# Performance work log

Measured on AMD Instinct MI355X. Metric: run time of the kernel, lower is better.

Reference implementation:

```python
import jax, jax.numpy as jnp
import numpy as np

D_MODEL = 1024
N_HEAD = 16
D_K = D_MODEL // N_HEAD
D_FF = 2048
N_EXPERTS = 8
TOP_K = 2
B = 4
S = 1024
LN_EPS = 1e-5


def _layer_norm(x, g, b):
    mu = jnp.mean(x, axis=-1, keepdims=True)
    var = jnp.mean(jnp.square(x - mu), axis=-1, keepdims=True)
    return (x - mu) * jax.lax.rsqrt(var + LN_EPS) * g + b


def setup_inputs() -> dict:
    key = jax.random.key(0)
    ks = jax.random.split(key, 16)
    std = 0.02
    inp = {
        "x": jax.random.normal(ks[0], (B, S, D_MODEL), dtype=jnp.float32),
        "mask": jnp.ones((B, S, S), dtype=jnp.int32),
        "ln1_g": jnp.ones((D_MODEL,), jnp.float32),
        "ln1_b": jnp.zeros((D_MODEL,), jnp.float32),
        "wq": jax.random.normal(ks[1], (D_MODEL, D_MODEL), jnp.float32) * std,
        "wk": jax.random.normal(ks[2], (D_MODEL, D_MODEL), jnp.float32) * std,
        "wv": jax.random.normal(ks[3], (D_MODEL, D_MODEL), jnp.float32) * std,
        "wo": jax.random.normal(ks[4], (D_MODEL, D_MODEL), jnp.float32) * std,
        "wqd": jax.random.normal(ks[5], (D_MODEL, D_MODEL), jnp.float32) * std,
        "wkd": jax.random.normal(ks[6], (D_MODEL, D_MODEL), jnp.float32) * std,
        "wvd": jax.random.normal(ks[7], (D_MODEL, D_MODEL), jnp.float32) * std,
        "wod": jax.random.normal(ks[8], (D_MODEL, D_MODEL), jnp.float32) * std,
        "w_gate": jax.random.normal(ks[9], (D_MODEL, 2), jnp.float32) * std,
        "ln2_g": jnp.ones((D_MODEL,), jnp.float32),
        "ln2_b": jnp.zeros((D_MODEL,), jnp.float32),
        "w_router": jax.random.normal(ks[10], (D_MODEL, N_EXPERTS), jnp.float32) * std,
        "e_w1": jax.random.normal(ks[11], (N_EXPERTS, D_MODEL, D_FF), jnp.float32) * std,
        "e_w2": jax.random.normal(ks[12], (N_EXPERTS, D_FF, D_MODEL), jnp.float32) * std,
    }
    return inp


def _attention(x, mask, wq, wk, wv, wo, wqd, wkd, wvd, wod, w_gate):
    b, s, d = x.shape

    def split_heads(t):  # [b,s,d] -> [b,h,s,dk]
        return t.reshape(b, s, N_HEAD, D_K).transpose(0, 2, 1, 3)

    def merge_heads(t):  # [b,h,s,dk] -> [b,s,d]
        return t.transpose(0, 2, 1, 3).reshape(b, s, d)

    # dense attention branch
    q = split_heads(x @ wq)
    k = split_heads(x @ wk)
    v = split_heads(x @ wv)
    scores = jnp.einsum("bhqd,bhkd->bhqk", q, k) / jnp.sqrt(jnp.float32(D_K))
    scores = jnp.where(mask[:, None, :, :] == 0, jnp.float32(-1e9), scores)
    probs = jax.nn.softmax(scores, axis=-1)
    dense = merge_heads(jnp.einsum("bhqk,bhkd->bhqd", probs, v)) @ wo

    # linear delta attention branch (O(n))
    qd = split_heads(x @ wqd)
    kd = split_heads(x @ wkd)
    vd = split_heads(x @ wvd)
    q_lin = jax.nn.relu(qd)
    k_lin = jax.nn.relu(kd)
    # NOTE: original uses the *non-relu* k for the context matrix
    context = jnp.einsum("bhsd,bhse->bhde", kd, vd)  # [b,h,dk,dk]
    out = jnp.einsum("bhsd,bhde->bhse", q_lin, context)
    z = jnp.sum(q_lin * jnp.sum(k_lin, axis=-2, keepdims=True), axis=-1, keepdims=True) + 1e-6
    delta = merge_heads(out / z) @ wod

    gate = jax.nn.softmax(x @ w_gate, axis=-1)  # [b,s,2]
    return gate[..., 0:1] * dense + gate[..., 1:2] * delta


def _moe(x, w_router, e_w1, e_w2):
    b, s, d = x.shape
    xt = x.reshape(b * s, d)  # tokens
    logits = xt @ w_router  # [N, E]
    topk_logits, topk_idx = jax.lax.top_k(logits, TOP_K)
    topk_w = jax.nn.softmax(topk_logits, axis=-1)  # [N, K]
    # dense combine weights [N, E] (equivalent to masked gather/scatter-add)
    n = xt.shape[0]
    comb = jnp.zeros((n, N_EXPERTS), xt.dtype).at[jnp.arange(n)[:, None], topk_idx].add(topk_w)
    # all tokens through all experts (jit-friendly dense dispatch)
    h = jax.nn.gelu(jnp.einsum("nd,edf->enf", xt, e_w1), approximate=False)
    y = jnp.einsum("enf,efd->end", h, e_w2)
    out = jnp.einsum("end,ne->nd", y, comb)
    return out.reshape(b, s, d)


def reference(x, mask, ln1_g, ln1_b, wq, wk, wv, wo, wqd, wkd, wvd, wod, w_gate,
              ln2_g, ln2_b, w_router, e_w1, e_w2):
    x = x + _attention(_layer_norm(x, ln1_g, ln1_b), mask,
                       wq, wk, wv, wo, wqd, wkd, wvd, wod, w_gate)
    x = x + _moe(_layer_norm(x, ln2_g, ln2_b), w_router, e_w1, e_w2)
    return x
```

## Files before the change

kernel.cpp:

```cpp
#include <hip/hip_runtime.h>
#include <stdint.h>


typedef __attribute__((ext_vector_type(8))) short short8;
typedef __attribute__((ext_vector_type(4))) float floatx4;

#define DMODEL 1024
#define SEQ    1024
#define NHEAD  16
#define DK     64
#define DFF    2048
#define NEXP   8
#define MAXTILE 144

__device__ __forceinline__ float bf2f(unsigned short h){
  union{unsigned u;float f;}v; v.u=((unsigned)h)<<16; return v.f;
}
__device__ __forceinline__ unsigned short f2bf(float f){
  union{float f;unsigned u;}v; v.f=f;
  unsigned r=(v.u + 0x7FFFu + ((v.u>>16)&1u))>>16; return (unsigned short)r;
}
__device__ __forceinline__ void splitbf(float v, unsigned short& hi, unsigned short& lo){
  hi = f2bf(v); lo = f2bf(v - bf2f(hi));
}

__device__ __forceinline__ void glds16(const unsigned short* g, unsigned short* l){
  __builtin_amdgcn_global_load_lds(
      (const __attribute__((address_space(1))) void*)g,
      (__attribute__((address_space(3))) void*)l, 16, 0, 0);
}

__device__ __forceinline__ float block_sum(float v, float* red){
  for(int off=32;off;off>>=1) v += __shfl_down(v,off,64);
  int w = threadIdx.x>>6;
  __syncthreads();
  if((threadIdx.x&63)==0) red[w]=v;
  __syncthreads();
  return red[0]+red[1]+red[2]+red[3];
}

__global__ __launch_bounds__(256) void k_maskpack(
    const int* __restrict__ mask, unsigned long long* __restrict__ mp){
  int gw = blockIdx.x*4 + (threadIdx.x>>6);
  int lane = threadIdx.x&63;
  unsigned long long bm = __ballot(mask[(long)gw*64 + lane] != 0);
  if(lane==0) mp[gw]=bm;
}

__global__ __launch_bounds__(256) void k_transpose_f2(
    const float* __restrict__ src, unsigned short* __restrict__ dh,
    unsigned short* __restrict__ dl, long srs, long drs, long sbs, long dbs){
  __shared__ float t[32][33];
  src += (long)blockIdx.z*sbs; dh += (long)blockIdx.z*dbs; dl += (long)blockIdx.z*dbs;
  int c0 = blockIdx.x*32, r0 = blockIdx.y*32;
  int tx = threadIdx.x & 31, ty = threadIdx.x >> 5;
  for(int i=0;i<32;i+=8)
    t[ty+i][tx] = src[(long)(r0+ty+i)*srs + (c0+tx)];
  __syncthreads();
  for(int i=0;i<32;i+=8){
    unsigned short hi,lo; splitbf(t[tx][ty+i],hi,lo);
    long idx = (long)(c0+ty+i)*drs + (r0+tx);
    dh[idx]=hi; dl[idx]=lo;
  }
}

__global__ __launch_bounds__(256) void k_transpose_f(
    const float* __restrict__ src, unsigned short* __restrict__ dst,
    long srs, long drs, long sbs, long dbs){
  __shared__ float t[32][33];
  src += (long)blockIdx.z*sbs; dst += (long)blockIdx.z*dbs;
  int c0 = blockIdx.x*32, r0 = blockIdx.y*32;
  int tx = threadIdx.x & 31, ty = threadIdx.x >> 5;
  for(int i=0;i<32;i+=8)
    t[ty+i][tx] = src[(long)(r0+ty+i)*srs + (c0+tx)];
  __syncthreads();
  for(int i=0;i<32;i+=8)
    dst[(long)(c0+ty+i)*drs + (r0+tx)] = f2bf(t[tx][ty+i]);
}

__global__ __launch_bounds__(256) void k_vt(
    const unsigned short* __restrict__ qh, const unsigned short* __restrict__ ql,
    unsigned short* __restrict__ vth, unsigned short* __restrict__ vtl, long coff){
  __shared__ unsigned short th[32][33], tl[32][33];
  int z = blockIdx.z, b = z>>4, h = z&15;
  int s0 = blockIdx.x*32, d0 = blockIdx.y*32;
  int tx = threadIdx.x & 31, ty = threadIdx.x >> 5;
  for(int i=0;i<32;i+=8){
    long src = (long)(b*SEQ + s0+ty+i)*6144 + coff + h*DK + d0+tx;
    th[ty+i][tx] = qh[src]; tl[ty+i][tx] = ql[src];
  }
  __syncthreads();
  for(int i=0;i<32;i+=8){
    long dst = ((long)z*DK + d0+ty+i)*SEQ + s0+tx;
    vth[dst] = th[tx][ty+i]; vtl[dst] = tl[tx][ty+i];
  }
}

__global__ __launch_bounds__(256) void k_ln1(
    const float* __restrict__ x, const float* __restrict__ g,
    const float* __restrict__ b, unsigned short* __restrict__ oh,
    unsigned short* __restrict__ ol){
  __shared__ float red[4];
  int t = blockIdx.x, tid = threadIdx.x;
  long base = (long)t*DMODEL + tid*4;
  floatx4 xv = *(const floatx4*)(x + base);
  float v[4] = {xv[0], xv[1], xv[2], xv[3]};
  float s = block_sum(v[0]+v[1]+v[2]+v[3], red);
  float mu = s * (1.f/DMODEL);
  float q=0.f;
  for(int i=0;i<4;i++){ float d=v[i]-mu; q+=d*d; }
  q = block_sum(q, red);
  float inv = rsqrtf(q*(1.f/DMODEL) + 1e-5f);
  for(int i=0;i<4;i++){
    int d = tid*4+i;
    unsigned short hi,lo; splitbf((v[i]-mu)*inv*g[d] + b[d], hi, lo);
    oh[base+i]=hi; ol[base+i]=lo;
  }
}

template<int SPLIT>
__global__ __launch_bounds__(256) void k_gemm128_ss(
    const unsigned short* __restrict__ Ah, const unsigned short* __restrict__ Al,
    const unsigned short* __restrict__ Bh, const unsigned short* __restrict__ Bl,
    unsigned short* __restrict__ Ch, unsigned short* __restrict__ Cl,
    float* __restrict__ Cf, int K, int lda, int ldb, int ldc, int gridN){
  __shared__ unsigned short Ash[128*32], Asl[128*32];
  __shared__ unsigned short Bsh[128*32], Bsl[128*32];
  int nwg = gridDim.x, bid = blockIdx.x;
  int swz = (bid & 7)*(nwg >> 3) + (bid >> 3);
  int bx = swz % gridN, by = swz / gridN;
  int m0 = by*128, n0 = bx*128;
  int tid = threadIdx.x, w = tid>>6, lane = tid&63;
  int qm = lane&15, quad = lane>>4;
  int wr = w>>1, wc = w&1;
  int lg = lane>>3, pp = lane&7, px = pp ^ lg;
  int rowl = (w<<4) + (lg<<1) + (px>>2);
  int c4s = (px&3)*8;
  int sdst = w*512 + lane*8;
  const unsigned short* pA0h = Ah + (long)(m0+rowl   )*lda + c4s;
  const unsigned short* pA1h = Ah + (long)(m0+rowl+64)*lda + c4s;
  const unsigned short* pA0l = Al + (long)(m0+rowl   )*lda + c4s;
  const unsigned short* pA1l = Al + (long)(m0+rowl+64)*lda + c4s;
  const unsigned short* pB0h = Bh + (long)(n0+rowl   )*ldb + c4s;
  const unsigned short* pB1h = Bh + (long)(n0+rowl+64)*ldb + c4s;
  const unsigned short* pB0l = Bl + (long)(n0+rowl   )*ldb + c4s;
  const unsigned short* pB1l = Bl + (long)(n0+rowl+64)*ldb + c4s;
  int fc = (((((qm&1)<<2)|quad) ^ (qm>>1))<<3);

  floatx4 acc[4][4];
  #pragma unroll
  for(int m=0;m<4;m++)
    #pragma unroll
    for(int n=0;n<4;n++) acc[m][n] = (floatx4){0.f,0.f,0.f,0.f};

  for(int k0=0;k0<K;k0+=32){
    __syncthreads();
    glds16(pA0h+k0, Ash+sdst); glds16(pA1h+k0, Ash+sdst+2048);
    glds16(pA0l+k0, Asl+sdst); glds16(pA1l+k0, Asl+sdst+2048);
    glds16(pB0h+k0, Bsh+sdst); glds16(pB1h+k0, Bsh+sdst+2048);
    glds16(pB0l+k0, Bsl+sdst); glds16(pB1l+k0, Bsl+sdst+2048);
    __syncthreads();
    short8 ah[4], al[4], bh[4], bl[4];
    #pragma unroll
    for(int m=0;m<4;m++){
      int ar = (wr*32 + m*8 + (qm>>1))*64 + fc;
      ah[m] = *(const short8*)(Ash+ar);
      al[m] = *(const short8*)(Asl+ar);
    }
    #pragma unroll
    for(int n=0;n<4;n++){
      int br = (wc*32 + n*8 + (qm>>1))*64 + fc;
      bh[n] = *(const short8*)(Bsh+br);
      bl[n] = *(const short8*)(Bsl+br);
    }
    #pragma unroll
    for(int m=0;m<4;m++)
      #pragma unroll
      for(int n=0;n<4;n++){
        acc[m][n] = __builtin_amdgcn_mfma_f32_16x16x32_bf16(ah[m],bh[n],acc[m][n],0,0,0);
        acc[m][n] = __builtin_amdgcn_mfma_f32_16x16x32_bf16(ah[m],bl[n],acc[m][n],0,0,0);
        acc[m][n] = __builtin_amdgcn_mfma_f32_16x16x32_bf16(al[m],bh[n],acc[m][n],0,0,0);
      }
  }
  #pragma unroll
  for(int m=0;m<4;m++){
    int row = m0 + wr*64 + m*16 + quad*4;
    #pragma unroll
    for(int r=0;r<4;r++){
      long rb = (long)(row+r)*ldc + n0 + wc*64;
      #pragma unroll
      for(int n=0;n<4;n++){
        float v = acc[m][n][r];
        if(SPLIT){
          unsigned short hi,lo; splitbf(v,hi,lo);
          Ch[rb+n*16+qm]=hi; Cl[rb+n*16+qm]=lo;
        }else{
          Cf[rb+n*16+qm]=v;
        }
      }
    }
  }
}

__global__ __launch_bounds__(256) void k_gate(
    const unsigned short* __restrict__ hh, const unsigned short* __restrict__ hl,
    const float* __restrict__ wg, float* __restrict__ gates){
  int token = blockIdx.x*4 + (threadIdx.x>>6);
  int lane = threadIdx.x&63;
  long hb = (long)token*DMODEL + lane*16;
  const float* w = wg + lane*16*2;
  float s0=0.f, s1=0.f;
  for(int i=0;i<16;i++){
    float hv = bf2f(hh[hb+i]) + bf2f(hl[hb+i]);
    s0 += hv*w[2*i]; s1 += hv*w[2*i+1];
  }
  for(int off=32;off;off>>=1){ s0+=__shfl_down(s0,off,64); s1+=__shfl_down(s1,off,64); }
  if(lane==0){
    float m=fmaxf(s0,s1), e0=__expf(s0-m), e1=__expf(s1-m), inv=1.f/(e0+e1);
    gates[token*2]=e0*inv; gates[token*2+1]=e1*inv;
  }
}

__global__ __launch_bounds__(256) void k_attn_flash3(
    const unsigned short* __restrict__ qh, const unsigned short* __restrict__ qlp,
    const unsigned short* __restrict__ vth, const unsigned short* __restrict__ vtl,
    const unsigned long long* __restrict__ mp, unsigned short* __restrict__ dmh,
    unsigned short* __restrict__ dml){
  __shared__ unsigned short Ksh[64*64], Ksl[64*64];
  __shared__ unsigned short Vsh[64*64], Vsl[64*64];
  __shared__ unsigned short PWh[4*16*64], PWl[4*16*64];
  int bh = blockIdx.y, b = bh>>4, h = bh&15;
  int tid = threadIdx.x, w = tid>>6, lane = tid&63;
  int qm = lane&15, quad = (lane>>4)&3;
  int q0 = blockIdx.x*64 + w*16;
  long qrow = (long)(b*SEQ+q0+qm)*6144 + h*DK;
  short8 a_qh0 = *(const short8*)(qh +qrow+quad*8);
  short8 a_qh1 = *(const short8*)(qh +qrow+32+quad*8);
  short8 a_ql0 = *(const short8*)(qlp+qrow+quad*8);
  short8 a_ql1 = *(const short8*)(qlp+qrow+32+quad*8);
  float m[4], l[4];
  floatx4 o0={0,0,0,0}, o1={0,0,0,0}, o2={0,0,0,0}, o3={0,0,0,0};
  #pragma unroll
  for(int r=0;r<4;r++){ m[r]=-3.0e38f; l[r]=0.f; }
  const unsigned long long* mrow = mp + ((long)b*SEQ + q0 + quad*4)*16;

  int r8 = lane>>3;
  int c8 = (lane&7) ^ r8;
  int d0 = w*512 + lane*8;
  const unsigned short* pKh0 = qh  + (long)(b*SEQ + w*8 + r8)*6144 + 1024 + h*DK + c8*8;
  const unsigned short* pKl0 = qlp + (long)(b*SEQ + w*8 + r8)*6144 + 1024 + h*DK + c8*8;
  const unsigned short* pKh1 = pKh0 + 32L*6144;
  const unsigned short* pKl1 = pKl0 + 32L*6144;
  const unsigned short* pVh0 = vth + ((long)bh*DK + w*8 + r8)*SEQ + c8*8;
  const unsigned short* pVl0 = vtl + ((long)bh*DK + w*8 + r8)*SEQ + c8*8;
  const unsigned short* pVh1 = pVh0 + 32L*SEQ;
  const unsigned short* pVl1 = pVl0 + 32L*SEQ;
  int q7 = qm&7;

  for(int kt=0; kt<SEQ; kt+=64){
    __syncthreads();
    long ko = (long)kt*6144;
    glds16(pKh0+ko, Ksh+d0); glds16(pKh1+ko, Ksh+d0+2048);
    glds16(pKl0+ko, Ksl+d0); glds16(pKl1+ko, Ksl+d0+2048);
    glds16(pVh0+kt, Vsh+d0); glds16(pVh1+kt, Vsh+d0+2048);
    glds16(pVl0+kt, Vsl+d0); glds16(pVl1+kt, Vsl+d0+2048);
    __syncthreads();

    int wd = kt>>6;
    unsigned long long mws[4] = {mrow[wd], mrow[16+wd], mrow[32+wd], mrow[48+wd]};
    floatx4 s[4];
    #pragma unroll
    for(int st=0;st<4;st++){
      int krow = (st*16+qm)*64;
      short8 kh0 = *(const short8*)(Ksh + krow + ((quad    ^q7)<<3));
      short8 kh1 = *(const short8*)(Ksh + krow + (((4|quad)^q7)<<3));
      short8 kl0 = *(const short8*)(Ksl + krow + ((quad    ^q7)<<3));
      short8 kl1 = *(const short8*)(Ksl + krow + (((4|quad)^q7)<<3));
      floatx4 acc = {0,0,0,0};
      acc = __builtin_amdgcn_mfma_f32_16x16x32_bf16(a_qh0,kh0,acc,0,0,0);
      acc = __builtin_amdgcn_mfma_f32_16x16x32_bf16(a_qh1,kh1,acc,0,0,0);
      acc = __builtin_amdgcn_mfma_f32_16x16x32_bf16(a_qh0,kl0,acc,0,0,0);
      acc = __builtin_amdgcn_mfma_f32_16x16x32_bf16(a_qh1,kl1,acc,0,0,0);
      acc = __builtin_amdgcn_mfma_f32_16x16x32_bf16(a_ql0,kh0,acc,0,0,0);
      acc = __builtin_amdgcn_mfma_f32_16x16x32_bf16(a_ql1,kh1,acc,0,0,0);
      s[st] = acc;
    }
    #pragma unroll
    for(int r=0;r<4;r++){
      float v0 = ((mws[r]>>(   qm))&1) ? s[0][r]*0.125f : -1e9f;
      float v1 = ((mws[r]>>(16+qm))&1) ? s[1][r]*0.125f : -1e9f;
      float v2 = ((mws[r]>>(32+qm))&1) ? s[2][r]*0.125f : -1e9f;
      float v3 = ((mws[r]>>(48+qm))&1) ? s[3][r]*0.125f : -1e9f;
      float tm = fmaxf(fmaxf(v0,v1), fmaxf(v2,v3));
      tm = fmaxf(tm, __shfl_xor(tm,1,16));
      tm = fmaxf(tm, __shfl_xor(tm,2,16));
      tm = fmaxf(tm, __shfl_xor(tm,4,16));
      tm = fmaxf(tm, __shfl_xor(tm,8,16));
      float nm = fmaxf(m[r], tm);
      float al = __expf(m[r]-nm);
      m[r] = nm;
      float p0=__expf(v0-nm), p1=__expf(v1-nm), p2=__expf(v2-nm), p3=__expf(v3-nm);
      float rs = p0+p1+p2+p3;
      rs += __shfl_xor(rs,1,16); rs += __shfl_xor(rs,2,16);
      rs += __shfl_xor(rs,4,16); rs += __shfl_xor(rs,8,16);
      l[r] = l[r]*al + rs;
      o0[r]*=al; o1[r]*=al; o2[r]*=al; o3[r]*=al;
      int row = quad*4+r, rsw = row&7;
      int pb = w*1024 + row*64 + (qm&7);
      unsigned short hi,lo;
      splitbf(p0,hi,lo); PWh[pb + ((( (qm>>3))^rsw)<<3)]=hi; PWl[pb + ((( (qm>>3))^rsw)<<3)]=lo;
      splitbf(p1,hi,lo); PWh[pb + (((2|(qm>>3))^rsw)<<3)]=hi; PWl[pb + (((2|(qm>>3))^rsw)<<3)]=lo;
      splitbf(p2,hi,lo); PWh[pb + (((4|(qm>>3))^rsw)<<3)]=hi; PWl[pb + (((4|(qm>>3))^rsw)<<3)]=lo;
      splitbf(p3,hi,lo); PWh[pb + (((6|(qm>>3))^rsw)<<3)]=hi; PWl[pb + (((6|(qm>>3))^rsw)<<3)]=lo;
    }
    __builtin_amdgcn_wave_barrier();
    int prb = w*1024 + qm*64;
    short8 ph0 = *(const short8*)(PWh + prb + ((quad    ^q7)<<3));
    short8 ph1 = *(const short8*)(PWh + prb + (((4|quad)^q7)<<3));
    short8 pl0 = *(const short8*)(PWl + prb + ((quad    ^q7)<<3));
    short8 pl1 = *(const short8*)(PWl + prb + (((4|quad)^q7)<<3));
    __builtin_amdgcn_wave_barrier();
    {
      int c0 = (quad    ^q7)<<3;
      int c1 = ((4|quad)^q7)<<3;
      int vr0 = (0*16+qm)*64, vr1 = (1*16+qm)*64, vr2 = (2*16+qm)*64, vr3 = (3*16+qm)*64;
      short8 v0h0=*(const short8*)(Vsh+vr0+c0), v0h1=*(const short8*)(Vsh+vr0+c1);
      short8 v1h0=*(const short8*)(Vsh+vr1+c0), v1h1=*(const short8*)(Vsh+vr1+c1);
      short8 v2h0=*(const short8*)(Vsh+vr2+c0), v2h1=*(const short8*)(Vsh+vr2+c1);
      short8 v3h0=*(const short8*)(Vsh+vr3+c0), v3h1=*(const short8*)(Vsh+vr3+c1);
      short8 v0l0=*(const short8*)(Vsl+vr0+c0), v0l1=*(const short8*)(Vsl+vr0+c1);
      short8 v1l0=*(const short8*)(Vsl+vr1+c0), v1l1=*(const short8*)(Vsl+vr1+c1);
      short8 v2l0=*(const short8*)(Vsl+vr2+c0), v2l1=*(const short8*)(Vsl+vr2+c1);
      short8 v3l0=*(const short8*)(Vsl+vr3+c0), v3l1=*(const short8*)(Vsl+vr3+c1);
      o0 = __builtin_amdgcn_mfma_f32_16x16x32_bf16(ph0,v0h0,o0,0,0,0);
      o0 = __builtin_amdgcn_mfma_f32_16x16x32_bf16(ph1,v0h1,o0,0,0,0);
      o0 = __builtin_amdgcn_mfma_f32_16x16x32_bf16(ph0,v0l0,o0,0,0,0);
      o0 = __builtin_amdgcn_mfma_f32_16x16x32_bf16(ph1,v0l1,o0,0,0,0);
      o0 = __builtin_amdgcn_mfma_f32_16x16x32_bf16(pl0,v0h0,o0,0,0,0);
      o0 = __builtin_amdgcn_mfma_f32_16x16x32_bf16(pl1,v0h1,o0,0,0,0);
      o1 = __builtin_amdgcn_mfma_f32_16x16x32_bf16(ph0,v1h0,o1,0,0,0);
      o1 = __builtin_amdgcn_mfma_f32_16x16x32_bf16(ph1,v1h1,o1,0,0,0);
      o1 = __builtin_amdgcn_mfma_f32_16x16x32_bf16(ph0,v1l0,o1,0,0,0);
      o1 = __builtin_amdgcn_mfma_f32_16x16x32_bf16(ph1,v1l1,o1,0,0,0);
      o1 = __builtin_amdgcn_mfma_f32_16x16x32_bf16(pl0,v1h0,o1,0,0,0);
      o1 = __builtin_amdgcn_mfma_f32_16x16x32_bf16(pl1,v1h1,o1,0,0,0);
      o2 = __builtin_amdgcn_mfma_f32_16x16x32_bf16(ph0,v2h0,o2,0,0,0);
      o2 = __builtin_amdgcn_mfma_f32_16x16x32_bf16(ph1,v2h1,o2,0,0,0);
      o2 = __builtin_amdgcn_mfma_f32_16x16x32_bf16(ph0,v2l0,o2,0,0,0);
      o2 = __builtin_amdgcn_mfma_f32_16x16x32_bf16(ph1,v2l1,o2,0,0,0);
      o2 = __builtin_amdgcn_mfma_f32_16x16x32_bf16(pl0,v2h0,o2,0,0,0);
      o2 = __builtin_amdgcn_mfma_f32_16x16x32_bf16(pl1,v2h1,o2,0,0,0);
      o3 = __builtin_amdgcn_mfma_f32_16x16x32_bf16(ph0,v3h0,o3,0,0,0);
      o3 = __builtin_amdgcn_mfma_f32_16x16x32_bf16(ph1,v3h1,o3,0,0,0);
      o3 = __builtin_amdgcn_mfma_f32_16x16x32_bf16(ph0,v3l0,o3,0,0,0);
      o3 = __builtin_amdgcn_mfma_f32_16x16x32_bf16(ph1,v3l1,o3,0,0,0);
      o3 = __builtin_amdgcn_mfma_f32_16x16x32_bf16(pl0,v3h0,o3,0,0,0);
      o3 = __builtin_amdgcn_mfma_f32_16x16x32_bf16(pl1,v3h1,o3,0,0,0);
    }
  }
  #pragma unroll
  for(int r=0;r<4;r++){
    float inv = 1.f/l[r];
    long rb = ((long)(b*SEQ + q0 + quad*4 + r))*DMODEL + h*DK;
    unsigned short hi,lo;
    splitbf(o0[r]*inv,hi,lo); dmh[rb+   qm]=hi; dml[rb+   qm]=lo;
    splitbf(o1[r]*inv,hi,lo); dmh[rb+16+qm]=hi; dml[rb+16+qm]=lo;
    splitbf(o2[r]*inv,hi,lo); dmh[rb+32+qm]=hi; dml[rb+32+qm]=lo;
    splitbf(o3[r]*inv,hi,lo); dmh[rb+48+qm]=hi; dml[rb+48+qm]=lo;
  }
}

__global__ __launch_bounds__(256) void k_delta_ctx2(
    const unsigned short* __restrict__ kdTh, const unsigned short* __restrict__ kdTl,
    const unsigned short* __restrict__ vdTh, const unsigned short* __restrict__ vdTl,
    float* __restrict__ ctx){
  int bh = blockIdx.x;
  int tid = threadIdx.x, w = tid>>6, lane = tid&63;
  int qm = lane&15, quad = lane>>4;
  long abase = ((long)bh*DK + w*16 + qm)*SEQ + quad*8;
  long bbase = ((long)bh*DK + qm)*SEQ + quad*8;
  floatx4 acc[4];
  #pragma unroll
  for(int n=0;n<4;n++) acc[n] = (floatx4){0.f,0.f,0.f,0.f};
  #pragma unroll 2
  for(int s0=0;s0<SEQ;s0+=32){
    short8 ah = *(const short8*)(kdTh + abase + s0);
    short8 al = *(const short8*)(kdTl + abase + s0);
    #pragma unroll
    for(int n=0;n<4;n++){
      short8 bh8 = *(const short8*)(vdTh + bbase + (long)n*16*SEQ + s0);
      short8 bl8 = *(const short8*)(vdTl + bbase + (long)n*16*SEQ + s0);
      acc[n] = __builtin_amdgcn_mfma_f32_16x16x32_bf16(ah,bh8,acc[n],0,0,0);
      acc[n] = __builtin_amdgcn_mfma_f32_16x16x32_bf16(ah,bl8,acc[n],0,0,0);
      acc[n] = __builtin_amdgcn_mfma_f32_16x16x32_bf16(al,bh8,acc[n],0,0,0);
    }
  }
  long cb = (long)bh*DK*DK;
  #pragma unroll
  for(int n=0;n<4;n++)
    #pragma unroll
    for(int r=0;r<4;r++)
      ctx[cb + (long)(w*16 + quad*4 + r)*DK + n*16 + qm] = acc[n][r];
}

__global__ __launch_bounds__(256) void k_ksum(
    const unsigned short* __restrict__ kdTh, const unsigned short* __restrict__ kdTl,
    float* __restrict__ ksum){
  int bh = blockIdx.x, tid = threadIdx.x;
  int d = tid>>2, part = tid&3;
  long base = ((long)bh*DK + d)*SEQ + part*256;
  float s = 0.f;
  for(int i=0;i<256;i+=8){
    short8 hq = *(const short8*)(kdTh+base+i);
    short8 lq = *(const short8*)(kdTl+base+i);
    #pragma unroll
    for(int j=0;j<8;j++)
      s += fmaxf(bf2f((unsigned short)hq[j]) + bf2f((unsigned short)lq[j]), 0.f);
  }
  s += __shfl_xor(s,1,64); s += __shfl_xor(s,2,64);
  if(part==0) ksum[bh*DK + d] = s;
}

__global__ __launch_bounds__(256) void k_delta_out(
    const unsigned short* __restrict__ qh, const unsigned short* __restrict__ qlp,
    const float* __restrict__ ctx, const float* __restrict__ ksum,
    unsigned short* __restrict__ dlh, unsigned short* __restrict__ dll){
  int tok = blockIdx.x, b = tok>>10;
  int tid = threadIdx.x;
  __shared__ float ql[DMODEL];
  long sb = (long)tok*6144 + 3072;
  for(int c=tid;c<DMODEL;c+=256)
    ql[c] = fmaxf(bf2f(qh[sb+c]) + bf2f(qlp[sb+c]), 0.f);
  __syncthreads();
  int h = tid>>4, dg = (tid&15)*4;
  int bh = b*NHEAD + h;
  const float* C = ctx + (long)bh*DK*DK;
  const float* KS = ksum + bh*DK;
  float a0=0,a1=0,a2=0,a3=0,z=0;
  for(int d=0;d<DK;d++){
    float q = ql[h*DK + d];
    z += q * KS[d];
    const float* cr = C + d*DK + dg;
    a0 += q*cr[0]; a1 += q*cr[1]; a2 += q*cr[2]; a3 += q*cr[3];
  }
  float inv = 1.f/(z + 1e-6f);
  long db = (long)tok*DMODEL + h*DK + dg;
  unsigned short hi,lo;
  splitbf(a0*inv,hi,lo); dlh[db  ]=hi; dll[db  ]=lo;
  splitbf(a1*inv,hi,lo); dlh[db+1]=hi; dll[db+1]=lo;
  splitbf(a2*inv,hi,lo); dlh[db+2]=hi; dll[db+2]=lo;
  splitbf(a3*inv,hi,lo); dlh[db+3]=hi; dll[db+3]=lo;
}

__global__ __launch_bounds__(256) void k_comb_router(
    const float* __restrict__ x, const float* __restrict__ dp,
    const float* __restrict__ dlp, const float* __restrict__ gates,
    const float* __restrict__ g, const float* __restrict__ bb,
    const float* __restrict__ wr, unsigned short* __restrict__ h2b,
    float* __restrict__ topw, int* __restrict__ topi, int* __restrict__ counts){
  __shared__ float red[4];
  __shared__ float ered[4][8];
  int t = blockIdx.x, tid = threadIdx.x;
  float g0 = gates[t*2], g1 = gates[t*2+1];
  long base = (long)t*DMODEL + tid*4;
  floatx4 xv = *(const floatx4*)(x + base);
  float v[4];
  for(int i=0;i<4;i++) v[i] = xv[i] + g0*dp[base+i] + g1*dlp[base+i];
  float s = block_sum(v[0]+v[1]+v[2]+v[3], red);
  float mu = s*(1.f/DMODEL);
  float q=0.f; for(int i=0;i<4;i++){ float d=v[i]-mu; q+=d*d; }
  q = block_sum(q, red);
  float inv = rsqrtf(q*(1.f/DMODEL)+1e-5f);
  float a[8]; for(int e=0;e<8;e++) a[e]=0.f;
  for(int i=0;i<4;i++){
    int d = tid*4+i;
    float hv = (v[i]-mu)*inv*g[d] + bb[d];
    h2b[base+i] = f2bf(hv);
    const float* wrow = wr + (long)d*NEXP;
    for(int e=0;e<8;e++) a[e] += hv*wrow[e];
  }
  for(int off=32;off;off>>=1)
    for(int e=0;e<8;e++) a[e] += __shfl_down(a[e],off,64);
  int w = tid>>6;
  if((tid&63)==0) for(int e=0;e<8;e++) ered[w][e]=a[e];
  __syncthreads();
  if(tid==0){
    float lg[8];
    for(int e=0;e<8;e++) lg[e]=ered[0][e]+ered[1][e]+ered[2][e]+ered[3][e];
    int i0=0; for(int e=1;e<8;e++) if(lg[e]>lg[i0]) i0=e;
    int i1=-1; for(int e=0;e<8;e++){ if(e==i0) continue; if(i1<0||lg[e]>lg[i1]) i1=e; }
    float mm=fmaxf(lg[i0],lg[i1]), e0=__expf(lg[i0]-mm), e1=__expf(lg[i1]-mm), s2=1.f/(e0+e1);
    topw[t*2]=e0*s2; topw[t*2+1]=e1*s2;
    topi[t*2]=i0; topi[t*2+1]=i1;
    atomicAdd(&counts[i0],1); atomicAdd(&counts[i1],1);
  }
}

__global__ void k_meta(const int* __restrict__ counts, int* offs, int* tE,
                       int* tR0, int* tR1, int* ntp, int* cursor){
  if(threadIdx.x==0){
    int o=0, nt=0;
    for(int e=0;e<NEXP;e++){
      offs[e]=o; cursor[e]=0;
      int n=counts[e];
      for(int t=0;t<(n+127)/128;t++){ tE[nt]=e; tR0[nt]=o+t*128; tR1[nt]=o+n; nt++; }
      o+=n;
    }
    offs[NEXP]=o; ntp[0]=nt;
  }
}

__global__ __launch_bounds__(256) void k_scatter(
    const int* __restrict__ topi, const int* __restrict__ offs,
    int* cursor, int* perm, int* slotof){
  int token = blockIdx.x*256 + threadIdx.x;
  for(int k=0;k<2;k++){
    int e = topi[token*2+k];
    int pos = atomicAdd(&cursor[e],1);
    int slot = offs[e]+pos;
    perm[slot]=token; slotof[token*2+k]=slot;
  }
}

template<int GELU, int GATHER>
__global__ __launch_bounds__(256) void k_moe128(
    const unsigned short* __restrict__ A, const unsigned short* __restrict__ BtA,
    unsigned short* __restrict__ C, const int* __restrict__ perm,
    const int* __restrict__ ntp, const int* __restrict__ tE,
    const int* __restrict__ tR0, const int* __restrict__ tR1,
    int K, int N){
  int bz = blockIdx.y;
  if(bz >= ntp[0]) return;
  int e = tE[bz], r0t = tR0[bz], r1t = tR1[bz];
  __shared__ unsigned short As[128*32], Bs[128*32];
  int tid = threadIdx.x, w = tid>>6, lane = tid&63;
  int qm = lane&15, quad = lane>>4;
  int wr = w>>1, wc = w&1;
  int n0 = blockIdx.x*128;
  int lg = lane>>3, pp = lane&7, px = pp ^ lg;
  int rowl = (w<<4) + (lg<<1) + (px>>2);
  int c4s = (px&3)*8;
  int sdst = w*512 + lane*8;
  int fc = (((((qm&1)<<2)|quad) ^ (qm>>1))<<3);
  int gr0 = r0t + rowl, gr1 = gr0 + 64;
  int gc0 = gr0 < 8191 ? gr0 : 8191;
  int gc1 = gr1 < 8191 ? gr1 : 8191;
  const unsigned short* pA0;
  const unsigned short* pA1;
  if(GATHER){
    pA0 = A + (long)perm[gc0]*K + c4s;
    pA1 = A + (long)perm[gc1]*K + c4s;
  }else{
    pA0 = A + (long)gc0*K + c4s;
    pA1 = A + (long)gc1*K + c4s;
  }
  const unsigned short* Bt = BtA + (long)e*N*K;
  const unsigned short* pB0 = Bt + (long)(n0+rowl   )*K + c4s;
  const unsigned short* pB1 = Bt + (long)(n0+rowl+64)*K + c4s;

  floatx4 acc[4][4];
  #pragma unroll
  for(int m=0;m<4;m++)
    #pragma unroll
    for(int n=0;n<4;n++) acc[m][n] = (floatx4){0.f,0.f,0.f,0.f};

  for(int k0=0;k0<K;k0+=32){
    __syncthreads();
    glds16(pA0+k0, As+sdst); glds16(pA1+k0, As+sdst+2048);
    glds16(pB0+k0, Bs+sdst); glds16(pB1+k0, Bs+sdst+2048);
    __syncthreads();
    short8 af[4], bf[4];
    #pragma unroll
    for(int m=0;m<4;m++)
      af[m] = *(const short8*)(As + (wr*32 + m*8 + (qm>>1))*64 + fc);
    #pragma unroll
    for(int n=0;n<4;n++)
      bf[n] = *(const short8*)(Bs + (wc*32 + n*8 + (qm>>1))*64 + fc);
    #pragma unroll
    for(int m=0;m<4;m++)
      #pragma unroll
      for(int n=0;n<4;n++)
        acc[m][n] = __builtin_amdgcn_mfma_f32_16x16x32_bf16(af[m],bf[n],acc[m][n],0,0,0);
  }
  #pragma unroll
  for(int m=0;m<4;m++){
    int row = r0t + wr*64 + m*16 + quad*4;
    #pragma unroll
    for(int r=0;r<4;r++){
      if(row+r < r1t){
        long rb = (long)(row+r)*N + n0 + wc*64;
        #pragma unroll
        for(int n=0;n<4;n++){
          float xx = acc[m][n][r];
          if(GELU) xx = 0.5f*xx*(1.f+erff(xx*0.70710678f));
          C[rb+n*16+qm] = f2bf(xx);
        }
      }
    }
  }
}

__global__ __launch_bounds__(256) void k_final(
    const float* __restrict__ x, const float* __restrict__ dp,
    const float* __restrict__ dlp, const float* __restrict__ gates,
    const unsigned short* __restrict__ Y, const int* __restrict__ slotof,
    const float* __restrict__ topw, float* __restrict__ out){
  int t = blockIdx.x, tid = threadIdx.x;
  int s0 = slotof[t*2], s1 = slotof[t*2+1];
  float w0 = topw[t*2], w1 = topw[t*2+1];
  float g0 = gates[t*2], g1 = gates[t*2+1];
  long base = (long)t*DMODEL + tid*4;
  const unsigned short* y0 = Y + (long)s0*DMODEL + tid*4;
  const unsigned short* y1 = Y + (long)s1*DMODEL + tid*4;
  floatx4 xv = *(const floatx4*)(x + base);
  for(int i=0;i<4;i++)
    out[base+i] = xv[i] + g0*dp[base+i] + g1*dlp[base+i]
                        + w0*bf2f(y0[i]) + w1*bf2f(y1[i]);
}

extern "C" void kernel_launch(void* const* d_in, const int* in_sizes, int n_in,
                              void* d_out, int out_size, void* d_ws, size_t ws_size,
                              hipStream_t stream){
  const float* x    = (const float*)d_in[0];
  const int*   mask = (const int*)d_in[1];
  const float* ln1g = (const float*)d_in[2];
  const float* ln1b = (const float*)d_in[3];
  const float* wq   = (const float*)d_in[4];
  const float* wk   = (const float*)d_in[5];
  const float* wv   = (const float*)d_in[6];
  const float* wo   = (const float*)d_in[7];
  const float* wqd  = (const float*)d_in[8];
  const float* wkd  = (const float*)d_in[9];
  const float* wvd  = (const float*)d_in[10];
  const float* wod  = (const float*)d_in[11];
  const float* wg   = (const float*)d_in[12];
  const float* ln2g = (const float*)d_in[13];
  const float* ln2b = (const float*)d_in[14];
  const float* wr   = (const float*)d_in[15];
  const float* ew1  = (const float*)d_in[16];
  const float* ew2  = (const float*)d_in[17];
  float* out = (float*)d_out;

  char* p = (char*)d_ws;
  auto alloc = [&](size_t b)->char*{ char* r=p; p += (b + 255) & ~(size_t)255; return r; };
  unsigned short* WtAllh = (unsigned short*)alloc(6144L*1024*2);
  unsigned short* WtAlll = (unsigned short*)alloc(6144L*1024*2);
  unsigned short* WoTh   = (unsigned short*)alloc(1024L*1024*2);
  unsigned short* WoTl   = (unsigned short*)alloc(1024L*1024*2);
  unsigned short* WodTh  = (unsigned short*)alloc(1024L*1024*2);
  unsigned short* WodTl  = (unsigned short*)alloc(1024L*1024*2);
  unsigned short* eW1T   = (unsigned short*)alloc(8L*2048*1024*2);
  unsigned short* eW2T   = (unsigned short*)alloc(8L*1024*2048*2);
  unsigned short* h1h    = (unsigned short*)alloc(4096L*1024*2);
  unsigned short* h1l    = (unsigned short*)alloc(4096L*1024*2);
  unsigned short* qkvh   = (unsigned short*)alloc(4096L*6144*2);
  unsigned short* qkvl   = (unsigned short*)alloc(4096L*6144*2);
  unsigned short* dmh    = (unsigned short*)alloc(4096L*1024*2);
  unsigned short* dml    = (unsigned short*)alloc(4096L*1024*2);
  unsigned short* dlh    = (unsigned short*)alloc(4096L*1024*2);
  unsigned short* dll    = (unsigned short*)alloc(4096L*1024*2);
  float* ctx   = (float*)alloc(64L*64*64*4);
  float* ksum  = (float*)alloc(64L*64*4);
  float* gates = (float*)alloc(4096L*2*4);
  unsigned short* h2b = (unsigned short*)alloc(4096L*1024*2);
  float* topw = (float*)alloc(4096L*2*4);
  int* topi   = (int*)alloc(4096L*2*4);
  int* slotof = (int*)alloc(4096L*2*4);
  int* perm   = (int*)alloc(8192L*4);
  int* counts = (int*)alloc(64*4);
  int* cursor = (int*)alloc(64*4);
  int* offs   = (int*)alloc(64*4);
  int* ntp    = (int*)alloc(64*4);
  int* tE     = (int*)alloc(MAXTILE*4);
  int* tR0    = (int*)alloc(MAXTILE*4);
  int* tR1    = (int*)alloc(MAXTILE*4);
  unsigned long long* mpack = (unsigned long long*)alloc(4L*1024*16*8);
  if ((size_t)(p - (char*)d_ws) > ws_size) return;

  unsigned short* vTh = h1h;
  unsigned short* vTl = h1l;
  unsigned short* kdTh = dlh;
  unsigned short* kdTl = dll;
  unsigned short* vdTh = dmh;
  unsigned short* vdTl = dml;
  float* dproj  = (float*)qkvh;
  float* dlproj = (float*)(qkvh + 8388608);
  unsigned short* H = qkvl;
  unsigned short* Y = dmh;

  dim3 tb(256);
  k_maskpack<<<16384,tb,0,stream>>>(mask, mpack);
  k_transpose_f2<<<dim3(32,32,1),tb,0,stream>>>(wq,  WtAllh+0L*1048576, WtAlll+0L*1048576, 1024,1024, 0,0);
  k_transpose_f2<<<dim3(32,32,1),tb,0,stream>>>(wk,  WtAllh+1L*1048576, WtAlll+1L*1048576, 1024,1024, 0,0);
  k_transpose_f2<<<dim3(32,32,1),tb,0,stream>>>(wv,  WtAllh+2L*1048576, WtAlll+2L*1048576, 1024,1024, 0,0);
  k_transpose_f2<<<dim3(32,32,1),tb,0,stream>>>(wqd, WtAllh+3L*1048576, WtAlll+3L*1048576, 1024,1024, 0,0);
  k_transpose_f2<<<dim3(32,32,1),tb,0,stream>>>(wkd, WtAllh+4L*1048576, WtAlll+4L*1048576, 1024,1024, 0,0);
  k_transpose_f2<<<dim3(32,32,1),tb,0,stream>>>(wvd, WtAllh+5L*1048576, WtAlll+5L*1048576, 1024,1024, 0,0);
  k_transpose_f2<<<dim3(32,32,1),tb,0,stream>>>(wo,  WoTh,  WoTl,  1024,1024, 0,0);
  k_transpose_f2<<<dim3(32,32,1),tb,0,stream>>>(wod, WodTh, WodTl, 1024,1024, 0,0);
  k_transpose_f<<<dim3(64,32,8),tb,0,stream>>>(ew1, eW1T, 2048,1024, 1024L*2048, 2048L*1024);
  k_transpose_f<<<dim3(32,64,8),tb,0,stream>>>(ew2, eW2T, 1024,2048, 2048L*1024, 1024L*2048);
  k_ln1<<<4096,tb,0,stream>>>(x, ln1g, ln1b, h1h, h1l);
  k_gemm128_ss<1><<<dim3(1536),tb,0,stream>>>(h1h,h1l, WtAllh,WtAlll, qkvh,qkvl,nullptr,
                                              1024, 1024, 1024, 6144, 48);
  k_gate<<<1024,tb,0,stream>>>(h1h, h1l, wg, gates);
  k_vt<<<dim3(32,2,64),tb,0,stream>>>(qkvh, qkvl, vTh, vTl, 2048);
  k_vt<<<dim3(32,2,64),tb,0,stream>>>(qkvh, qkvl, kdTh, kdTl, 4096);
  k_vt<<<dim3(32,2,64),tb,0,stream>>>(qkvh, qkvl, vdTh, vdTl, 5120);
  k_delta_ctx2<<<64,tb,0,stream>>>(kdTh, kdTl, vdTh, vdTl, ctx);
  k_ksum<<<64,tb,0,stream>>>(kdTh, kdTl, ksum);
  k_attn_flash3<<<dim3(16,64),tb,0,stream>>>(qkvh, qkvl, vTh, vTl, mpack, dmh, dml);
  k_delta_out<<<4096,tb,0,stream>>>(qkvh, qkvl, ctx, ksum, dlh, dll);
  k_gemm128_ss<0><<<dim3(256),tb,0,stream>>>(dmh,dml, WoTh,WoTl,  nullptr,nullptr,dproj,
                                             1024, 1024, 1024, 1024, 8);
  k_gemm128_ss<0><<<dim3(256),tb,0,stream>>>(dlh,dll, WodTh,WodTl, nullptr,nullptr,dlproj,
                                             1024, 1024, 1024, 1024, 8);
  hipMemsetAsync(counts, 0, NEXP*sizeof(int), stream);
  k_comb_router<<<4096,tb,0,stream>>>(x, dproj, dlproj, gates, ln2g, ln2b, wr,
                                      h2b, topw, topi, counts);
  k_meta<<<1,64,0,stream>>>(counts, offs, tE, tR0, tR1, ntp, cursor);
  k_scatter<<<16,tb,0,stream>>>(topi, offs, cursor, perm, slotof);
  k_moe128<1,1><<<dim3(16,72),tb,0,stream>>>(h2b, eW1T, H, perm, ntp, tE, tR0, tR1,
                                             1024, 2048);
  k_moe128<0,0><<<dim3(8,72),tb,0,stream>>>(H, eW2T, Y, perm, ntp, tE, tR0, tR1,
                                            2048, 1024);
  k_final<<<4096,tb,0,stream>>>(x, dproj, dlproj, gates, Y, slotof, topw, out);
}
```

Baseline: 1.060 ms.

## Fuse transposes, ksum into ctx, dual output projections, widen MoE tiles

Merges the three V/Kd/Vd transpose launches into one kernel and folds the ReLU key-sum into the delta context kernel, so the separate ksum kernel goes away. Replaces the two output-projection GEMMs with a single 512-block kernel that covers both. Widens the MoE expert GEMM tiles from 128 to 256 columns to reuse each A tile across more outputs. This cuts launch count and redundant reads, but the larger MoE tiles double the accumulator registers and shared memory and halve the grid, which may lower occupancy.

```diff
diff --git a/kernel.cpp b/kernel.cpp
--- a/kernel.cpp
+++ b/kernel.cpp
@@ -78,12 +78,18 @@
     dst[(long)(c0+ty+i)*drs + (r0+tx)] = f2bf(t[tx][ty+i]);
 }
 
-__global__ __launch_bounds__(256) void k_vt(
+__global__ __launch_bounds__(256) void k_vt3(
     const unsigned short* __restrict__ qh, const unsigned short* __restrict__ ql,
-    unsigned short* __restrict__ vth, unsigned short* __restrict__ vtl, long coff){
+    unsigned short* __restrict__ vTh, unsigned short* __restrict__ vTl,
+    unsigned short* __restrict__ kdTh, unsigned short* __restrict__ kdTl,
+    unsigned short* __restrict__ vdTh, unsigned short* __restrict__ vdTl){
   __shared__ unsigned short th[32][33], tl[32][33];
   int z = blockIdx.z, b = z>>4, h = z&15;
-  int s0 = blockIdx.x*32, d0 = blockIdx.y*32;
+  int slice = blockIdx.y >> 1;
+  long coff = (slice==0) ? 2048 : (slice==1 ? 4096 : 5120);
+  unsigned short* dh = (slice==0) ? vTh : (slice==1 ? kdTh : vdTh);
+  unsigned short* dl = (slice==0) ? vTl : (slice==1 ? kdTl : vdTl);
+  int s0 = blockIdx.x*32, d0 = (blockIdx.y&1)*32;
   int tx = threadIdx.x & 31, ty = threadIdx.x >> 5;
   for(int i=0;i<32;i+=8){
     long src = (long)(b*SEQ + s0+ty+i)*6144 + coff + h*DK + d0+tx;
@@ -92,7 +98,7 @@
   __syncthreads();
   for(int i=0;i<32;i+=8){
     long dst = ((long)z*DK + d0+ty+i)*SEQ + s0+tx;
-    vth[dst] = th[tx][ty+i]; vtl[dst] = tl[tx][ty+i];
+    dh[dst] = th[tx][ty+i]; dl[dst] = tl[tx][ty+i];
   }
 }
 
@@ -198,6 +204,89 @@
           Cf[rb+n*16+qm]=v;
         }
       }
+    }
+  }
+}
+
+__global__ __launch_bounds__(256) void k_proj2(
+    const unsigned short* __restrict__ dmh, const unsigned short* __restrict__ dml,
+    const unsigned short* __restrict__ dlh, const unsigned short* __restrict__ dll,
+    const unsigned short* __restrict__ WoTh, const unsigned short* __restrict__ WoTl,
+    const unsigned short* __restrict__ WodTh, const unsigned short* __restrict__ WodTl,
+    float* __restrict__ dproj, float* __restrict__ dlproj){
+  __shared__ unsigned short Ash[128*32], Asl[128*32];
+  __shared__ unsigned short Bsh[128*32], Bsl[128*32];
+  int bid = blockIdx.x;
+  int swz = (bid & 7)*64 + (bid >> 3);
+  int which = swz >> 8, rem = swz & 255;
+  int bx = rem & 7, by = rem >> 3;
+  int m0 = by*128, n0 = bx*128;
+  const unsigned short* Ah = which ? dlh : dmh;
+  const unsigned short* Al = which ? dll : dml;
+  const unsigned short* Bh = which ? WodTh : WoTh;
+  const unsigned short* Bl = which ? WodTl : WoTl;
+  float* Cf = which ? dlproj : dproj;
+  int tid = threadIdx.x, w = tid>>6, lane = tid&63;
+  int qm = lane&15, quad = lane>>4;
+  int wr = w>>1, wc = w&1;
+  int lg = lane>>3, pp = lane&7, px = pp ^ lg;
+  int rowl = (w<<4) + (lg<<1) + (px>>2);
+  int c4s = (px&3)*8;
+  int sdst = w*512 + lane*8;
+  const unsigned short* pA0h = Ah + (long)(m0+rowl   )*1024 + c4s;
+  const unsigned short* pA1h = Ah + (long)(m0+rowl+64)*1024 + c4s;
+  const unsigned short* pA0l = Al + (long)(m0+rowl   )*1024 + c4s;
+  const unsigned short* pA1l = Al + (long)(m0+rowl+64)*1024 + c4s;
+  const unsigned short* pB0h = Bh + (long)(n0+rowl   )*1024 + c4s;
+  const unsigned short* pB1h = Bh + (long)(n0+rowl+64)*1024 + c4s;
+  const unsigned short* pB0l = Bl + (long)(n0+rowl   )*1024 + c4s;
+  const unsigned short* pB1l = Bl + (long)(n0+rowl+64)*1024 + c4s;
+  int fc = (((((qm&1)<<2)|quad) ^ (qm>>1))<<3);
+
+  floatx4 acc[4][4];
+  #pragma unroll
+  for(int m=0;m<4;m++)
+    #pragma unroll
+    for(int n=0;n<4;n++) acc[m][n] = (floatx4){0.f,0.f,0.f,0.f};
+
+  for(int k0=0;k0<1024;k0+=32){
+    __syncthreads();
+    glds16(pA0h+k0, Ash+sdst); glds16(pA1h+k0, Ash+sdst+2048);
+    glds16(pA0l+k0, Asl+sdst); glds16(pA1l+k0, Asl+sdst+2048);
+    glds16(pB0h+k0, Bsh+sdst); glds16(pB1h+k0, Bsh+sdst+2048);
+    glds16(pB0l+k0, Bsl+sdst); glds16(pB1l+k0, Bsl+sdst+2048);
+    __syncthreads();
+    short8 ah[4], al[4], bh[4], bl[4];
+    #pragma unroll
+    for(int m=0;m<4;m++){
+      int ar = (wr*32 + m*8 + (qm>>1))*64 + fc;
+      ah[m] = *(const short8*)(Ash+ar);
+      al[m] = *(const short8*)(Asl+ar);
+    }
+    #pragma unroll
+    for(int n=0;n<4;n++){
+      int br = (wc*32 + n*8 + (qm>>1))*64 + fc;
+      bh[n] = *(const short8*)(Bsh+br);
+      bl[n] = *(const short8*)(Bsl+br);
+    }
+    #pragma unroll
+    for(int m=0;m<4;m++)
+      #pragma unroll
+      for(int n=0;n<4;n++){
+        acc[m][n] = __builtin_amdgcn_mfma_f32_16x16x32_bf16(ah[m],bh[n],acc[m][n],0,0,0);
+        acc[m][n] = __builtin_amdgcn_mfma_f32_16x16x32_bf16(ah[m],bl[n],acc[m][n],0,0,0);
+        acc[m][n] = __builtin_amdgcn_mfma_f32_16x16x32_bf16(al[m],bh[n],acc[m][n],0,0,0);
+      }
+  }
+  #pragma unroll
+  for(int m=0;m<4;m++){
+    int row = m0 + wr*64 + m*16 + quad*4;
+    #pragma unroll
+    for(int r=0;r<4;r++){
+      long rb = (long)(row+r)*1024 + n0 + wc*64;
+      #pragma unroll
+      for(int n=0;n<4;n++)
+        Cf[rb+n*16+qm] = acc[m][n][r];
     }
   }
 }
@@ -373,7 +462,7 @@
 __global__ __launch_bounds__(256) void k_delta_ctx2(
     const unsigned short* __restrict__ kdTh, const unsigned short* __restrict__ kdTl,
     const unsigned short* __restrict__ vdTh, const unsigned short* __restrict__ vdTl,
-    float* __restrict__ ctx){
+    float* __restrict__ ctx, float* __restrict__ ksum){
   int bh = blockIdx.x;
   int tid = threadIdx.x, w = tid>>6, lane = tid&63;
   int qm = lane&15, quad = lane>>4;
@@ -382,10 +471,14 @@
   floatx4 acc[4];
   #pragma unroll
   for(int n=0;n<4;n++) acc[n] = (floatx4){0.f,0.f,0.f,0.f};
+  float ks = 0.f;
   #pragma unroll 2
   for(int s0=0;s0<SEQ;s0+=32){
     short8 ah = *(const short8*)(kdTh + abase + s0);
     short8 al = *(const short8*)(kdTl + abase + s0);
+    #pragma unroll
+    for(int j=0;j<8;j++)
+      ks += fmaxf(bf2f((unsigned short)ah[j]) + bf2f((unsigned short)al[j]), 0.f);
     #pragma unroll
     for(int n=0;n<4;n++){
       short8 bh8 = *(const short8*)(vdTh + bbase + (long)n*16*SEQ + s0);
@@ -401,24 +494,9 @@
     #pragma unroll
     for(int r=0;r<4;r++)
       ctx[cb + (long)(w*16 + quad*4 + r)*DK + n*16 + qm] = acc[n][r];
-}
-
-__global__ __launch_bounds__(256) void k_ksum(
-    const unsigned short* __restrict__ kdTh, const unsigned short* __restrict__ kdTl,
-    float* __restrict__ ksum){
-  int bh = blockIdx.x, tid = threadIdx.x;
-  int d = tid>>2, part = tid&3;
-  long base = ((long)bh*DK + d)*SEQ + part*256;
-  float s = 0.f;
-  for(int i=0;i<256;i+=8){
-    short8 hq = *(const short8*)(kdTh+base+i);
-    short8 lq = *(const short8*)(kdTl+base+i);
-    #pragma unroll
-    for(int j=0;j<8;j++)
-      s += fmaxf(bf2f((unsigned short)hq[j]) + bf2f((unsigned short)lq[j]), 0.f);
-  }
-  s += __shfl_xor(s,1,64); s += __shfl_xor(s,2,64);
-  if(part==0) ksum[bh*DK + d] = s;
+  ks += __shfl_xor(ks,16,64);
+  ks += __shfl_xor(ks,32,64);
+  if(quad==0) ksum[bh*DK + w*16 + qm] = ks;
 }
 
 __global__ __launch_bounds__(256) void k_delta_out(
@@ -523,7 +601,7 @@
 }
 
 template<int GELU, int GATHER>
-__global__ __launch_bounds__(256) void k_moe128(
+__global__ __launch_bounds__(256) void k_moe256(
     const unsigned short* __restrict__ A, const unsigned short* __restrict__ BtA,
     unsigned short* __restrict__ C, const int* __restrict__ perm,
     const int* __restrict__ ntp, const int* __restrict__ tE,
@@ -532,11 +610,11 @@
   int bz = blockIdx.y;
   if(bz >= ntp[0]) return;
   int e = tE[bz], r0t = tR0[bz], r1t = tR1[bz];
-  __shared__ unsigned short As[128*32], Bs[128*32];
+  __shared__ unsigned short As[128*32], Bs[256*32];
   int tid = threadIdx.x, w = tid>>6, lane = tid&63;
   int qm = lane&15, quad = lane>>4;
   int wr = w>>1, wc = w&1;
-  int n0 = blockIdx.x*128;
+  int n0 = blockIdx.x*256;
   int lg = lane>>3, pp = lane&7, px = pp ^ lg;
   int rowl = (w<<4) + (lg<<1) + (px>>2);
   int c4s = (px&3)*8;
@@ -545,8 +623,7 @@
   int gr0 = r0t + rowl, gr1 = gr0 + 64;
   int gc0 = gr0 < 8191 ? gr0 : 8191;
   int gc1 = gr1 < 8191 ? gr1 : 8191;
-  const unsigned short* pA0;
-  const unsigned short* pA1;
+  const unsigned short *pA0, *pA1;
   if(GATHER){
     pA0 = A + (long)perm[gc0]*K + c4s;
     pA1 = A + (long)perm[gc1]*K + c4s;
@@ -555,31 +632,34 @@
     pA1 = A + (long)gc1*K + c4s;
   }
   const unsigned short* Bt = BtA + (long)e*N*K;
-  const unsigned short* pB0 = Bt + (long)(n0+rowl   )*K + c4s;
-  const unsigned short* pB1 = Bt + (long)(n0+rowl+64)*K + c4s;
-
-  floatx4 acc[4][4];
+  const unsigned short* pB0 = Bt + (long)(n0+rowl    )*K + c4s;
+  const unsigned short* pB1 = Bt + (long)(n0+rowl+64 )*K + c4s;
+  const unsigned short* pB2 = Bt + (long)(n0+rowl+128)*K + c4s;
+  const unsigned short* pB3 = Bt + (long)(n0+rowl+192)*K + c4s;
+
+  floatx4 acc[4][8];
   #pragma unroll
   for(int m=0;m<4;m++)
     #pragma unroll
-    for(int n=0;n<4;n++) acc[m][n] = (floatx4){0.f,0.f,0.f,0.f};
+    for(int n=0;n<8;n++) acc[m][n] = (floatx4){0.f,0.f,0.f,0.f};
 
   for(int k0=0;k0<K;k0+=32){
     __syncthreads();
     glds16(pA0+k0, As+sdst); glds16(pA1+k0, As+sdst+2048);
-    glds16(pB0+k0, Bs+sdst); glds16(pB1+k0, Bs+sdst+2048);
+    glds16(pB0+k0, Bs+sdst);      glds16(pB1+k0, Bs+sdst+2048);
+    glds16(pB2+k0, Bs+sdst+4096); glds16(pB3+k0, Bs+sdst+6144);
     __syncthreads();
-    short8 af[4], bf[4];
+    short8 af[4], bf[8];
     #pragma unroll
     for(int m=0;m<4;m++)
       af[m] = *(const short8*)(As + (wr*32 + m*8 + (qm>>1))*64 + fc);
     #pragma unroll
-    for(int n=0;n<4;n++)
-      bf[n] = *(const short8*)(Bs + (wc*32 + n*8 + (qm>>1))*64 + fc);
+    for(int n=0;n<8;n++)
+      bf[n] = *(const short8*)(Bs + (wc*64 + n*8 + (qm>>1))*64 + fc);
     #pragma unroll
     for(int m=0;m<4;m++)
       #pragma unroll
-      for(int n=0;n<4;n++)
+      for(int n=0;n<8;n++)
         acc[m][n] = __builtin_amdgcn_mfma_f32_16x16x32_bf16(af[m],bf[n],acc[m][n],0,0,0);
   }
   #pragma unroll
@@ -588,9 +668,9 @@
     #pragma unroll
     for(int r=0;r<4;r++){
       if(row+r < r1t){
-        long rb = (long)(row+r)*N + n0 + wc*64;
+        long rb = (long)(row+r)*N + n0 + wc*128;
         #pragma unroll
-        for(int n=0;n<4;n++){
+        for(int n=0;n<8;n++){
           float xx = acc[m][n][r];
           if(GELU) xx = 0.5f*xx*(1.f+erff(xx*0.70710678f));
           C[rb+n*16+qm] = f2bf(xx);
@@ -704,25 +784,20 @@
   k_gemm128_ss<1><<<dim3(1536),tb,0,stream>>>(h1h,h1l, WtAllh,WtAlll, qkvh,qkvl,nullptr,
                                               1024, 1024, 1024, 6144, 48);
   k_gate<<<1024,tb,0,stream>>>(h1h, h1l, wg, gates);
-  k_vt<<<dim3(32,2,64),tb,0,stream>>>(qkvh, qkvl, vTh, vTl, 2048);
-  k_vt<<<dim3(32,2,64),tb,0,stream>>>(qkvh, qkvl, kdTh, kdTl, 4096);
-  k_vt<<<dim3(32,2,64),tb,0,stream>>>(qkvh, qkvl, vdTh, vdTl, 5120);
-  k_delta_ctx2<<<64,tb,0,stream>>>(kdTh, kdTl, vdTh, vdTl, ctx);
-  k_ksum<<<64,tb,0,stream>>>(kdTh, kdTl, ksum);
+  k_vt3<<<dim3(32,6,64),tb,0,stream>>>(qkvh, qkvl, vTh, vTl, kdTh, kdTl, vdTh, vdTl);
+  k_delta_ctx2<<<64,tb,0,stream>>>(kdTh, kdTl, vdTh, vdTl, ctx, ksum);
   k_attn_flash3<<<dim3(16,64),tb,0,stream>>>(qkvh, qkvl, vTh, vTl, mpack, dmh, dml);
   k_delta_out<<<4096,tb,0,stream>>>(qkvh, qkvl, ctx, ksum, dlh, dll);
-  k_gemm128_ss<0><<<dim3(256),tb,0,stream>>>(dmh,dml, WoTh,WoTl,  nullptr,nullptr,dproj,
-                                             1024, 1024, 1024, 1024, 8);
-  k_gemm128_ss<0><<<dim3(256),tb,0,stream>>>(dlh,dll, WodTh,WodTl, nullptr,nullptr,dlproj,
-                                             1024, 1024, 1024, 1024, 8);
+  k_proj2<<<dim3(512),tb,0,stream>>>(dmh,dml, dlh,dll, WoTh,WoTl, WodTh,WodTl,
+                                     dproj, dlproj);
   hipMemsetAsync(counts, 0, NEXP*sizeof(int), stream);
   k_comb_router<<<4096,tb,0,stream>>>(x, dproj, dlproj, gates, ln2g, ln2b, wr,
                                       h2b, topw, topi, counts);
   k_meta<<<1,64,0,stream>>>(counts, offs, tE, tR0, tR1, ntp, cursor);
   k_scatter<<<16,tb,0,stream>>>(topi, offs, cursor, perm, slotof);
-  k_moe128<1,1><<<dim3(16,72),tb,0,stream>>>(h2b, eW1T, H, perm, ntp, tE, tR0, tR1,
-                                             1024, 2048);
-  k_moe128<0,0><<<dim3(8,72),tb,0,stream>>>(H, eW2T, Y, perm, ntp, tE, tR0, tR1,
+  k_moe256<1,1><<<dim3(8,72),tb,0,stream>>>(h2b, eW1T, H, perm, ntp, tE, tR0, tR1,
+                                            1024, 2048);
+  k_moe256<0,0><<<dim3(4,72),tb,0,stream>>>(H, eW2T, Y, perm, ntp, tE, tR0, tR1,
                                             2048, 1024);
   k_final<<<4096,tb,0,stream>>>(x, dproj, dlproj, gates, Y, slotof, topw, out);
 }
```

Result: slower. 1.233 ms (+16.3%).
